# Kernel optimization log

Measured on AMD Instinct MI355X. Metric: run time of the kernel, lower is better.

Reference implementation:

```python
import jax, jax.numpy as jnp
import numpy as np

TAU = 2.0
V_TH = 1.0
V_RESET = 0.0
ALPHA = 2.0  # ATan surrogate alpha (spikingjelly default)

@jax.custom_vjp
def spike(x):
    # Heaviside forward, ATan surrogate backward
    return (x >= 0).astype(x.dtype)

def _spike_fwd(x):
    return spike(x), x

def _spike_bwd(x, g):
    pix = (jnp.pi / 2) * ALPHA * x
    return (g * (ALPHA / 2) / (1 + pix * pix),)

spike.defvjp(_spike_fwd, _spike_bwd)

def setup_inputs() -> dict:
    key = jax.random.key(0)
    k1, k2, k3 = jax.random.split(key, 3)
    T, B, I, H = 256, 128, 512, 512
    x = jax.random.normal(k1, (T, B, I), dtype=jnp.float32)
    W = jax.random.normal(k2, (H, I), dtype=jnp.float32) * (1.0 / np.sqrt(I))
    b = jax.random.normal(k3, (H,), dtype=jnp.float32) * 0.01
    return {"x": x, "W": W, "b": b}

def reference(x, W, b):
    # Linear projection over all timesteps at once: (T,B,I) @ (H,I)^T -> (T,B,H)
    h = jnp.einsum('tbi,hi->tbh', x, W) + b

    def step(v, ht):
        # LIFNode, decay_input=False, v_reset=0: charge, fire, hard reset
        v = v - (v - V_RESET) / TAU + ht
        s = spike(v - V_TH)
        s_d = jax.lax.stop_gradient(s)  # detach_reset=True
        v = v * (1.0 - s_d) + V_RESET * s_d
        return v, s

    v0 = jnp.zeros_like(h[0])
    _, spikes = jax.lax.scan(step, v0, h)
    # dropout_p=0 (inference) -> identity; no synapse filter
    return spikes
```

## Files before the change

kernel.cpp:

```cpp
#include <hip/hip_runtime.h>

#define T_STEPS 256
#define B_DIM   128
#define I_DIM   512
#define H_DIM   512
#define M_DIM   (T_STEPS * B_DIM)

#define BM 128
#define BN 128
#define BK 32
#define LDA (BM + 4)
#define LDB (BN + 4)

__global__ __launch_bounds__(256, 2) void gemm_bias_f32(
    const float* __restrict__ A,
    const float* __restrict__ Bw,
    const float* __restrict__ bias,
    float* __restrict__ C)
{
    __shared__ float As[BK][LDA];
    __shared__ float Bs[BK][LDB];

    const int tid = threadIdx.x;
    const int tx  = tid & 15;
    const int ty  = tid >> 4;
    const int m0  = blockIdx.y * BM;
    const int n0  = blockIdx.x * BN;

    float acc[8][8];
    #pragma unroll
    for (int i = 0; i < 8; i++)
        #pragma unroll
        for (int j = 0; j < 8; j++)
            acc[i][j] = 0.0f;

    const int lrow = tid >> 3;
    const int lk   = (tid & 7) * 4;

    const float* Aptr = A  + (size_t)(m0 + lrow) * I_DIM + lk;
    const float* Bptr = Bw + (size_t)(n0 + lrow) * I_DIM + lk;

    for (int k0 = 0; k0 < I_DIM; k0 += BK) {
        float4 av[4], bv[4];
        #pragma unroll
        for (int p = 0; p < 4; p++) {
            av[p] = *(const float4*)(Aptr + (size_t)(p * 32) * I_DIM + k0);
            bv[p] = *(const float4*)(Bptr + (size_t)(p * 32) * I_DIM + k0);
        }

        __syncthreads();

        #pragma unroll
        for (int p = 0; p < 4; p++) {
            const int r = lrow + p * 32;
            As[lk + 0][r] = av[p].x;
            As[lk + 1][r] = av[p].y;
            As[lk + 2][r] = av[p].z;
            As[lk + 3][r] = av[p].w;
            Bs[lk + 0][r] = bv[p].x;
            Bs[lk + 1][r] = bv[p].y;
            Bs[lk + 2][r] = bv[p].z;
            Bs[lk + 3][r] = bv[p].w;
        }

        __syncthreads();

        for (int k = 0; k < BK; k++) {
            float4 a0 = *(const float4*)&As[k][ty * 8];
            float4 a1 = *(const float4*)&As[k][ty * 8 + 4];
            float4 b0 = *(const float4*)&Bs[k][tx * 8];
            float4 b1 = *(const float4*)&Bs[k][tx * 8 + 4];
            float a[8] = {a0.x, a0.y, a0.z, a0.w, a1.x, a1.y, a1.z, a1.w};
            float b[8] = {b0.x, b0.y, b0.z, b0.w, b1.x, b1.y, b1.z, b1.w};
            #pragma unroll
            for (int i = 0; i < 8; i++)
                #pragma unroll
                for (int j = 0; j < 8; j++)
                    acc[i][j] = fmaf(a[i], b[j], acc[i][j]);
        }
    }

    float bcol[8];
    #pragma unroll
    for (int j = 0; j < 8; j++)
        bcol[j] = bias[n0 + tx * 8 + j];

    #pragma unroll
    for (int i = 0; i < 8; i++) {
        const int m = m0 + ty * 8 + i;
        float4 o0, o1;
        o0.x = acc[i][0] + bcol[0];
        o0.y = acc[i][1] + bcol[1];
        o0.z = acc[i][2] + bcol[2];
        o0.w = acc[i][3] + bcol[3];
        o1.x = acc[i][4] + bcol[4];
        o1.y = acc[i][5] + bcol[5];
        o1.z = acc[i][6] + bcol[6];
        o1.w = acc[i][7] + bcol[7];
        float* cp = C + (size_t)m * H_DIM + n0 + tx * 8;
        *(float4*)(cp)     = o0;
        *(float4*)(cp + 4) = o1;
    }
}

#define SCAN_UNROLL 16
__global__ __launch_bounds__(256) void lif_scan(
    const float* __restrict__ h,
    float* __restrict__ out)
{
    const int n   = B_DIM * H_DIM;
    const int idx = blockIdx.x * 256 + threadIdx.x;
    const float* hp = h + idx;
    float* op = out + idx;

    float v = 0.0f;
    for (int t0 = 0; t0 < T_STEPS; t0 += SCAN_UNROLL) {
        float hv[SCAN_UNROLL];
        #pragma unroll
        for (int i = 0; i < SCAN_UNROLL; i++)
            hv[i] = hp[(size_t)(t0 + i) * n];

        float s[SCAN_UNROLL];
        #pragma unroll
        for (int i = 0; i < SCAN_UNROLL; i++) {
            v = 0.5f * v + hv[i];
            const bool fire = (v >= 1.0f);
            s[i] = fire ? 1.0f : 0.0f;
            v    = fire ? 0.0f : v;
        }

        #pragma unroll
        for (int i = 0; i < SCAN_UNROLL; i++)
            op[(size_t)(t0 + i) * n] = s[i];
    }
}

extern "C" void kernel_launch(void* const* d_in, const int* in_sizes, int n_in,
                              void* d_out, int out_size, void* d_ws, size_t ws_size,
                              hipStream_t stream) {
    const float* x = (const float*)d_in[0];
    const float* W = (const float*)d_in[1];
    const float* b = (const float*)d_in[2];
    float* out = (float*)d_out;
    float* h   = (float*)d_ws;

    dim3 grid(H_DIM / BN, M_DIM / BM);
    gemm_bias_f32<<<grid, 256, 0, stream>>>(x, W, b, h);

    lif_scan<<<(B_DIM * H_DIM) / 256, 256, 0, stream>>>(h, out);
}
```

Before: 317.7 us.

## Swizzle GEMM shared tiles, raise occupancy, double-buffer LIF scan loads

Replaces the padded shared-memory tiles in the GEMM with an XOR-swizzled float4 layout, aimed at avoiding LDS bank conflicts without padding. The output columns are remapped so each thread writes two float4s 64 columns apart, which makes the stores coalesced. Launch bounds are raised to three blocks per SM. The LIF scan now double-buffers 32-step register chunks so the next loads overlap compute, and writes spikes with nontemporal stores. The tradeoff is higher register pressure from the larger scan buffers and the occupancy hint, which may cause spills.

```diff
diff --git a/kernel.cpp b/kernel.cpp
--- a/kernel.cpp
+++ b/kernel.cpp
@@ -9,17 +9,15 @@
 #define BM 128
 #define BN 128
 #define BK 32
-#define LDA (BM + 4)
-#define LDB (BN + 4)
 
-__global__ __launch_bounds__(256, 2) void gemm_bias_f32(
+__global__ __launch_bounds__(256, 3) void gemm_bias_f32(
     const float* __restrict__ A,
     const float* __restrict__ Bw,
     const float* __restrict__ bias,
     float* __restrict__ C)
 {
-    __shared__ float As[BK][LDA];
-    __shared__ float Bs[BK][LDB];
+    __shared__ float As[BK * BM];
+    __shared__ float Bs[BK * BN];
 
     const int tid = threadIdx.x;
     const int tx  = tid & 15;
@@ -36,6 +34,7 @@
 
     const int lrow = tid >> 3;
     const int lk   = (tid & 7) * 4;
+    const int q    = tid & 7;
 
     const float* Aptr = A  + (size_t)(m0 + lrow) * I_DIM + lk;
     const float* Bptr = Bw + (size_t)(n0 + lrow) * I_DIM + lk;
@@ -52,24 +51,28 @@
 
         #pragma unroll
         for (int p = 0; p < 4; p++) {
-            const int r = lrow + p * 32;
-            As[lk + 0][r] = av[p].x;
-            As[lk + 1][r] = av[p].y;
-            As[lk + 2][r] = av[p].z;
-            As[lk + 3][r] = av[p].w;
-            Bs[lk + 0][r] = bv[p].x;
-            Bs[lk + 1][r] = bv[p].y;
-            Bs[lk + 2][r] = bv[p].z;
-            Bs[lk + 3][r] = bv[p].w;
+            const int r    = lrow + p * 32;
+            const int base = (((r >> 2) ^ q) << 2) + (r & 3);
+            As[(lk + 0) * BM + base] = av[p].x;
+            As[(lk + 1) * BM + base] = av[p].y;
+            As[(lk + 2) * BM + base] = av[p].z;
+            As[(lk + 3) * BM + base] = av[p].w;
+            Bs[(lk + 0) * BN + base] = bv[p].x;
+            Bs[(lk + 1) * BN + base] = bv[p].y;
+            Bs[(lk + 2) * BN + base] = bv[p].z;
+            Bs[(lk + 3) * BN + base] = bv[p].w;
         }
 
         __syncthreads();
 
+        const float4* As4 = (const float4*)As;
+        const float4* Bs4 = (const float4*)Bs;
         for (int k = 0; k < BK; k++) {
-            float4 a0 = *(const float4*)&As[k][ty * 8];
-            float4 a1 = *(const float4*)&As[k][ty * 8 + 4];
-            float4 b0 = *(const float4*)&Bs[k][tx * 8];
-            float4 b1 = *(const float4*)&Bs[k][tx * 8 + 4];
+            const int rho = (k >> 2) & 7;
+            float4 a0 = As4[k * (BM / 4) + ((ty * 2)     ^ rho)];
+            float4 a1 = As4[k * (BM / 4) + ((ty * 2 + 1) ^ rho)];
+            float4 b0 = Bs4[k * (BN / 4) + (tx        ^ rho)];
+            float4 b1 = Bs4[k * (BN / 4) + ((16 + tx) ^ rho)];
             float a[8] = {a0.x, a0.y, a0.z, a0.w, a1.x, a1.y, a1.z, a1.w};
             float b[8] = {b0.x, b0.y, b0.z, b0.w, b1.x, b1.y, b1.z, b1.w};
             #pragma unroll
@@ -80,30 +83,28 @@
         }
     }
 
-    float bcol[8];
-    #pragma unroll
-    for (int j = 0; j < 8; j++)
-        bcol[j] = bias[n0 + tx * 8 + j];
+    float4 bc0 = *(const float4*)(bias + n0 + tx * 4);
+    float4 bc1 = *(const float4*)(bias + n0 + 64 + tx * 4);
 
     #pragma unroll
     for (int i = 0; i < 8; i++) {
         const int m = m0 + ty * 8 + i;
         float4 o0, o1;
-        o0.x = acc[i][0] + bcol[0];
-        o0.y = acc[i][1] + bcol[1];
-        o0.z = acc[i][2] + bcol[2];
-        o0.w = acc[i][3] + bcol[3];
-        o1.x = acc[i][4] + bcol[4];
-        o1.y = acc[i][5] + bcol[5];
-        o1.z = acc[i][6] + bcol[6];
-        o1.w = acc[i][7] + bcol[7];
-        float* cp = C + (size_t)m * H_DIM + n0 + tx * 8;
-        *(float4*)(cp)     = o0;
-        *(float4*)(cp + 4) = o1;
+        o0.x = acc[i][0] + bc0.x;
+        o0.y = acc[i][1] + bc0.y;
+        o0.z = acc[i][2] + bc0.z;
+        o0.w = acc[i][3] + bc0.w;
+        o1.x = acc[i][4] + bc1.x;
+        o1.y = acc[i][5] + bc1.y;
+        o1.z = acc[i][6] + bc1.z;
+        o1.w = acc[i][7] + bc1.w;
+        float* cp = C + (size_t)m * H_DIM + n0;
+        *(float4*)(cp + tx * 4)      = o0;
+        *(float4*)(cp + 64 + tx * 4) = o1;
     }
 }
 
-#define SCAN_UNROLL 16
+#define SCAN_U 32
 __global__ __launch_bounds__(256) void lif_scan(
     const float* __restrict__ h,
     float* __restrict__ out)
@@ -113,25 +114,41 @@
     const float* hp = h + idx;
     float* op = out + idx;
 
+    float bufA[SCAN_U], bufB[SCAN_U];
+
+    #pragma unroll
+    for (int i = 0; i < SCAN_U; i++)
+        bufA[i] = hp[(size_t)i * n];
+
     float v = 0.0f;
-    for (int t0 = 0; t0 < T_STEPS; t0 += SCAN_UNROLL) {
-        float hv[SCAN_UNROLL];
+    for (int t0 = 0; t0 < T_STEPS; t0 += 2 * SCAN_U) {
         #pragma unroll
-        for (int i = 0; i < SCAN_UNROLL; i++)
-            hv[i] = hp[(size_t)(t0 + i) * n];
+        for (int i = 0; i < SCAN_U; i++)
+            bufB[i] = hp[(size_t)(t0 + SCAN_U + i) * n];
 
-        float s[SCAN_UNROLL];
         #pragma unroll
-        for (int i = 0; i < SCAN_UNROLL; i++) {
-            v = 0.5f * v + hv[i];
+        for (int i = 0; i < SCAN_U; i++) {
+            v = fmaf(0.5f, v, bufA[i]);
             const bool fire = (v >= 1.0f);
-            s[i] = fire ? 1.0f : 0.0f;
-            v    = fire ? 0.0f : v;
+            __builtin_nontemporal_store(fire ? 1.0f : 0.0f,
+                                        op + (size_t)(t0 + i) * n);
+            v = fire ? 0.0f : v;
+        }
+
+        if (t0 + 2 * SCAN_U < T_STEPS) {
+            #pragma unroll
+            for (int i = 0; i < SCAN_U; i++)
+                bufA[i] = hp[(size_t)(t0 + 2 * SCAN_U + i) * n];
         }
 
         #pragma unroll
-        for (int i = 0; i < SCAN_UNROLL; i++)
-            op[(size_t)(t0 + i) * n] = s[i];
+        for (int i = 0; i < SCAN_U; i++) {
+            v = fmaf(0.5f, v, bufB[i]);
+            const bool fire = (v >= 1.0f);
+            __builtin_nontemporal_store(fire ? 1.0f : 0.0f,
+                                        op + (size_t)(t0 + SCAN_U + i) * n);
+            v = fire ? 0.0f : v;
+        }
     }
 }
 
```

Result: no change. 321.1 us (+1.1%).
